# Optimization experiments

Measured on AMD Instinct MI355X. Metric: run time of the kernel, lower is better.

## Reference

```python
import jax, jax.numpy as jnp
import numpy as np

INPUT_DIM = 512
HIDDEN_DIM = 1024


def glorot_normal(key, shape):
    fan_in, fan_out = shape[0], shape[1]
    std = jnp.sqrt(2.0 / (fan_in + fan_out))
    return std * jax.random.normal(key, shape, dtype=jnp.float32)


def setup_inputs() -> dict:
    key = jax.random.key(0)
    k1, k2, k3 = jax.random.split(key, 3)
    b, t = 32, 1024
    H = HIDDEN_DIM + INPUT_DIM
    x_btd = jax.random.normal(k1, (b, t, INPUT_DIM), dtype=jnp.float32)
    input_paddings = jnp.zeros((b, t), dtype=jnp.float32)
    kernel = glorot_normal(k2, (H, 4 * HIDDEN_DIM))  # [H, 4h]
    bias = jnp.zeros((4 * HIDDEN_DIM,), dtype=jnp.float32)
    h_init = glorot_normal(k3, (1, HIDDEN_DIM))
    return {"x_btd": x_btd, "input_paddings": input_paddings,
            "kernel": kernel, "bias": bias, "h_init": h_init}


def lstm_step(carry, x_bd, kernel, bias):
    h_bh, c_bh = carry
    x_bH = jnp.concatenate([x_bd, h_bh], axis=-1)          # [b, d+h]
    gate_out = jnp.einsum('bH,Hh->bh', x_bH, kernel) + bias  # [b, 4h]
    f, i, o, g = jnp.split(gate_out, 4, axis=-1)
    c_new = jax.nn.sigmoid(f) * c_bh + jax.nn.sigmoid(i) * jnp.tanh(g)
    h_new = jax.nn.sigmoid(o) * jnp.tanh(c_new)
    return (h_new, c_new), h_new


def reference(x_btd, input_paddings, kernel, bias, h_init) -> jnp.ndarray:
    del input_paddings
    b = x_btd.shape[0]
    h0 = jnp.tile(h_init, (b, 1))                # [b, h]
    c0 = jnp.zeros((b, HIDDEN_DIM), dtype=x_btd.dtype)
    x_tbd = jnp.transpose(x_btd, (1, 0, 2))      # [t, b, d]

    def step(carry, x_bd):
        return lstm_step(carry, x_bd, kernel, bias)

    _, h_tbh = jax.lax.scan(step, (h0, c0), x_tbd)
    return jnp.transpose(h_tbh, (1, 0, 2))       # [b, t, h]
```

## Files before the change

### kernel.cpp

```cpp
#include <hip/hip_runtime.h>


#define T_STEPS 1024
#define BATCH   32
#define DIN     512
#define HID     1024
#define KTOT    1536
#define NBLK    128
#define RSTR    68
#define REDW    (16*RSTR)
#define NSLOT   8
#define HSLOT   32768

typedef __attribute__((ext_vector_type(8))) short  short8;
typedef __attribute__((ext_vector_type(4))) float  floatx4;
typedef __attribute__((ext_vector_type(4))) unsigned int uintx4;
typedef __attribute__((ext_vector_type(4))) unsigned short ushort4_;

#define MFMA16(a,b,c) __builtin_amdgcn_mfma_f32_16x16x32_bf16(a, b, c, 0, 0, 0)

__device__ __forceinline__ unsigned short f2bf(float f) {
    unsigned u = __builtin_bit_cast(unsigned, f);
    u += 0x7FFFu + ((u >> 16) & 1u);
    return (unsigned short)(u >> 16);
}
__device__ __forceinline__ float sigf(float x) { return 1.f / (1.f + __expf(-x)); }
__device__ __forceinline__ float tanh_fast(float x) {
    float e = __expf(2.f * x);
    return 1.f - 2.f / (e + 1.f);
}
__device__ __forceinline__ unsigned cvt2(float a, float b) {
    unsigned r;
    asm("v_cvt_pk_bf16_f32 %0, %1, %2" : "=v"(r) : "v"(a), "v"(b));
    return r;
}

__device__ __forceinline__ floatx4 coh_load16f(const void* p) {
    floatx4 v;
    asm volatile("global_load_dwordx4 %0, %1, off sc1" : "=v"(v) : "v"(p));
    return v;
}
__device__ __forceinline__ void coh_store4u(void* p, unsigned v) {
    asm volatile("global_store_dword %0, %1, off sc1" :: "v"(p), "v"(v) : "memory");
}
__device__ __forceinline__ void wait_vm0() {
    asm volatile("s_waitcnt vmcnt(0)" ::: "memory");
}

__global__ __launch_bounds__(256) void prep_wt(const float* __restrict__ kern,
                                               unsigned short* __restrict__ wt) {
    __shared__ unsigned short tile[64][72];
    const int c0 = (blockIdx.x & 63) * 64;
    const int k0 = (blockIdx.x >> 6) * 64;
    const int cl = threadIdx.x & 63;
    const int kg = threadIdx.x >> 6;
    #pragma unroll
    for (int i = 0; i < 16; ++i) {
        int kl = kg * 16 + i;
        tile[cl][kl] = f2bf(kern[(k0 + kl) * 4096 + c0 + cl]);
    }
    __syncthreads();
    #pragma unroll
    for (int i = 0; i < 16; ++i) {
        int cc = kg * 16 + i;
        wt[(size_t)(c0 + cc) * KTOT + k0 + cl] = tile[cc][cl];
    }
}

__global__ __launch_bounds__(256) void prep_x(const float* __restrict__ x,
                                              unsigned short* __restrict__ xT) {
    const int row = blockIdx.x * 2 + (threadIdx.x >> 7);
    const int l   = threadIdx.x & 127;
    const int b = row >> 10, t = row & 1023;
    float4 v = ((const float4*)(x + (size_t)row * DIN))[l];
    ushort4_ o;
    o.x = f2bf(v.x); o.y = f2bf(v.y); o.z = f2bf(v.z); o.w = f2bf(v.w);
    *(ushort4_*)(xT + ((size_t)t * BATCH + b) * DIN + l * 4) = o;
}

__global__ __launch_bounds__(256) void init_h(const float* __restrict__ h_init,
                                              unsigned* __restrict__ hbuf_u) {
    const int idx = blockIdx.x * 256 + threadIdx.x;
    const int uu = idx & 1023;
    hbuf_u[idx] = __builtin_bit_cast(unsigned, h_init[uu]) & ~1u;
    hbuf_u[HSLOT + idx] = 1u;
}

__global__ __launch_bounds__(512, 2) void lstm_persist(
    const unsigned short* __restrict__ wt,
    const unsigned short* __restrict__ xT,
    float* __restrict__ hbuf,
    const float* __restrict__ bias,
    float* __restrict__ out)
{
    __shared__ float red[2][NSLOT][REDW];

    const int bk   = blockIdx.x;
    const int p    = bk >> 6;
    const int ug   = bk & 63;
    const int tid  = threadIdx.x;
    const int w    = tid >> 6;
    const int lane = tid & 63;
    const int lrow = lane & 15;
    const int kq   = lane >> 4;

    unsigned* hbuf_u = (unsigned*)hbuf;

    short8 wbx[2][4], wbh[4][4];
    #pragma unroll
    for (int nf = 0; nf < 4; ++nf) {
        const size_t gcol = (size_t)(nf * HID + ug * 16 + lrow) * KTOT;
        #pragma unroll
        for (int i = 0; i < 2; ++i)
            wbx[i][nf] = *(const short8*)(wt + gcol + w * 64 + i * 32 + kq * 8);
        #pragma unroll
        for (int j = 0; j < 4; ++j)
            wbh[j][nf] = *(const short8*)(wt + gcol + 512 + w * 128 + j * 32 + kq * 8);
    }

    const int pb = tid >> 4;
    const int pu = tid & 15;
    float bias_r[4], c_state = 0.f;
    if (tid < 256) {
        #pragma unroll
        for (int g = 0; g < 4; ++g) bias_r[g] = bias[g * HID + ug * 16 + pu];
    }

    const int hoff = (p * 16 + lrow) * HID + w * 128 + kq * 8;

    floatx4 xa[2];

    {
        const floatx4 zero = {0.f, 0.f, 0.f, 0.f};
        floatx4 acc[4] = {zero, zero, zero, zero};
        const unsigned short* xb = xT + (size_t)(p * 16 + lrow) * DIN;
        #pragma unroll
        for (int i = 0; i < 2; ++i) {
            short8 a = *(const short8*)(xb + w * 64 + i * 32 + kq * 8);
            #pragma unroll
            for (int nf = 0; nf < 4; ++nf) acc[nf] = MFMA16(a, wbx[i][nf], acc[nf]);
        }
        const unsigned short* xn = xT + ((size_t)1 * BATCH + p * 16 + lrow) * DIN;
        #pragma unroll
        for (int i = 0; i < 2; ++i)
            xa[i] = *(const floatx4*)(xn + w * 64 + i * 32 + kq * 8);

        floatx4 hf[4][2];
        #pragma unroll
        for (int j = 0; j < 4; ++j) {
            hf[j][0] = coh_load16f(hbuf + hoff + j * 32);
            hf[j][1] = coh_load16f(hbuf + hoff + j * 32 + 4);
        }
        wait_vm0();
        __builtin_amdgcn_sched_barrier(0);
        #pragma unroll
        for (int j = 0; j < 4; ++j) {
            union { short8 s; unsigned u[4]; } wa;
            wa.u[0] = cvt2(hf[j][0][0], hf[j][0][1]);
            wa.u[1] = cvt2(hf[j][0][2], hf[j][0][3]);
            wa.u[2] = cvt2(hf[j][1][0], hf[j][1][1]);
            wa.u[3] = cvt2(hf[j][1][2], hf[j][1][3]);
            #pragma unroll
            for (int nf = 0; nf < 4; ++nf) acc[nf] = MFMA16(wa.s, wbh[j][nf], acc[nf]);
        }
        #pragma unroll
        for (int nf = 0; nf < 4; ++nf)
            #pragma unroll
            for (int r = 0; r < 4; ++r)
                red[0][w][(kq * 4 + r) * RSTR + nf * 16 + lrow] = acc[nf][r];
    }

    for (int t = 0; t < T_STEPS; ++t) {
        __syncthreads();

        const float* rc = &red[t & 1][0][0];
        float*       rn = &red[(t + 1) & 1][0][0];
        const unsigned tg = ((unsigned)(t + 1) >> 1) & 1u;
        const int      so = ((t + 1) & 1) * HSLOT;

        if (tid < 256) {
            float gv[4];
            #pragma unroll
            for (int g = 0; g < 4; ++g) {
                float s = bias_r[g];
                #pragma unroll
                for (int wv = 0; wv < NSLOT; ++wv)
                    s += rc[wv * REDW + pb * RSTR + g * 16 + pu];
                gv[g] = s;
            }
            const float fg = sigf(gv[0]);
            const float ig = sigf(gv[1]);
            const float og = sigf(gv[2]);
            const float gg = tanh_fast(gv[3]);
            c_state = fg * c_state + ig * gg;
            const float hn = og * tanh_fast(c_state);

            if (t + 1 < T_STEPS) {
                wait_vm0();
                unsigned hv = (__builtin_bit_cast(unsigned, hn) & ~1u) | tg;
                coh_store4u(hbuf_u + so + (p * 16 + pb) * HID + ug * 16 + pu, hv);
            }
            out[(size_t)(p * 16 + pb) * (T_STEPS * HID) + (size_t)t * HID
                + ug * 16 + pu] = hn;
        }

        if (t + 1 == T_STEPS) break;

        const floatx4 zero = {0.f, 0.f, 0.f, 0.f};
        floatx4 acc[4] = {zero, zero, zero, zero};
        #pragma unroll
        for (int i = 0; i < 2; ++i) {
            short8 a = __builtin_bit_cast(short8, xa[i]);
            #pragma unroll
            for (int nf = 0; nf < 4; ++nf) acc[nf] = MFMA16(a, wbx[i][nf], acc[nf]);
        }
        if (t + 2 < T_STEPS) {
            const unsigned short* xn = xT + ((size_t)(t + 2) * BATCH + p * 16 + lrow) * DIN;
            #pragma unroll
            for (int i = 0; i < 2; ++i)
                xa[i] = *(const floatx4*)(xn + w * 64 + i * 32 + kq * 8);
        }

        if (tid >= 256) __builtin_amdgcn_s_sleep(12);
        const float* hb = hbuf + so + hoff;
        floatx4 hf[4][2];
        #pragma unroll
        for (int j = 0; j < 4; ++j) {
            hf[j][0] = coh_load16f(hb + j * 32);
            hf[j][1] = coh_load16f(hb + j * 32 + 4);
        }
        wait_vm0();
        __builtin_amdgcn_sched_barrier(0);
        unsigned stale = 0;
        #pragma unroll
        for (int j = 0; j < 4; ++j)
            #pragma unroll
            for (int c2 = 0; c2 < 2; ++c2) {
                uintx4 u = __builtin_bit_cast(uintx4, hf[j][c2]);
                unsigned fr = tg ? (u[0] & u[1] & u[2] & u[3])
                                 : ~(u[0] | u[1] | u[2] | u[3]);
                if (!(fr & 1u)) stale |= 1u << (j * 2 + c2);
            }
        while (__any((int)(stale != 0u))) {
            if (__all((int)(stale == 0xFFu)))
                __builtin_amdgcn_s_sleep(8);
            #pragma unroll
            for (int j = 0; j < 4; ++j)
                #pragma unroll
                for (int c2 = 0; c2 < 2; ++c2)
                    if (stale & (1u << (j * 2 + c2)))
                        hf[j][c2] = coh_load16f(hb + j * 32 + c2 * 4);
            wait_vm0();
            __builtin_amdgcn_sched_barrier(0);
            unsigned ns = 0;
            #pragma unroll
            for (int j = 0; j < 4; ++j)
                #pragma unroll
                for (int c2 = 0; c2 < 2; ++c2)
                    if (stale & (1u << (j * 2 + c2))) {
                        uintx4 u = __builtin_bit_cast(uintx4, hf[j][c2]);
                        unsigned fr = tg ? (u[0] & u[1] & u[2] & u[3])
                                         : ~(u[0] | u[1] | u[2] | u[3]);
                        if (!(fr & 1u)) ns |= 1u << (j * 2 + c2);
                    }
            stale = ns;
        }

        #pragma unroll
        for (int j = 0; j < 4; ++j) {
            union { short8 s; unsigned u[4]; } wa;
            wa.u[0] = cvt2(hf[j][0][0], hf[j][0][1]);
            wa.u[1] = cvt2(hf[j][0][2], hf[j][0][3]);
            wa.u[2] = cvt2(hf[j][1][0], hf[j][1][1]);
            wa.u[3] = cvt2(hf[j][1][2], hf[j][1][3]);
            #pragma unroll
            for (int nf = 0; nf < 4; ++nf) acc[nf] = MFMA16(wa.s, wbh[j][nf], acc[nf]);
        }

        #pragma unroll
        for (int nf = 0; nf < 4; ++nf)
            #pragma unroll
            for (int r = 0; r < 4; ++r)
                rn[w * REDW + (kq * 4 + r) * RSTR + nf * 16 + lrow] = acc[nf][r];
    }
}

extern "C" void kernel_launch(void* const* d_in, const int* in_sizes, int n_in,
                              void* d_out, int out_size, void* d_ws, size_t ws_size,
                              hipStream_t stream) {
    (void)in_sizes; (void)n_in; (void)out_size;
    const float* x      = (const float*)d_in[0];
    const float* kern   = (const float*)d_in[2];
    const float* bias   = (const float*)d_in[3];
    const float* h_init = (const float*)d_in[4];
    float* out = (float*)d_out;

    char* ws = (char*)d_ws;
    unsigned short* wt   = (unsigned short*)(ws);
    unsigned short* xT   = (unsigned short*)(ws + 12582912);
    float*          hbuf = (float*)(ws + 12582912 + 33554432);
    (void)ws_size;

    prep_wt<<<dim3(64 * 24), dim3(256), 0, stream>>>(kern, wt);
    prep_x<<<dim3(BATCH * T_STEPS / 2), dim3(256), 0, stream>>>(x, xT);
    init_h<<<dim3(128), dim3(256), 0, stream>>>(h_init, (unsigned*)hbuf);

    void* args[] = { &wt, &xT, &hbuf, &bias, &out };
    hipLaunchCooperativeKernel((const void*)lstm_persist, dim3(NBLK), dim3(512),
                               args, 0, stream);
}
```

Before: 5.227 ms.

## Specialize waves into input-projection and recurrent-polling groups with adaptive backoff

Splits the eight waves per block into two roles. Four waves compute only the x·W input projection with doubled K depth, and four waves handle the h·W recurrent part, polling the coherent h buffer with doubled K depth. The point is to take the x projection and x prefetch off the critical polling path and to replace the fixed sleep with an adaptive backoff sized by how many polling rounds were needed. It also drops the wait before the h store and lowers launch bounds to one block per SIMD-group, which allows more registers per wave for the larger weight tile. The catch is that the h waves now do twice the MFMA work on the serial critical path.

```diff
diff --git a/kernel.cpp b/kernel.cpp
--- a/kernel.cpp
+++ b/kernel.cpp
@@ -86,7 +86,7 @@
     hbuf_u[HSLOT + idx] = 1u;
 }
 
-__global__ __launch_bounds__(512, 2) void lstm_persist(
+__global__ __launch_bounds__(512, 1) void lstm_persist(
     const unsigned short* __restrict__ wt,
     const unsigned short* __restrict__ xT,
     float* __restrict__ hbuf,
@@ -99,23 +99,32 @@
     const int p    = bk >> 6;
     const int ug   = bk & 63;
     const int tid  = threadIdx.x;
-    const int w    = tid >> 6;
+    const int wave = tid >> 6;
     const int lane = tid & 63;
     const int lrow = lane & 15;
     const int kq   = lane >> 4;
+    const bool isG = wave < 4;
 
     unsigned* hbuf_u = (unsigned*)hbuf;
 
-    short8 wbx[2][4], wbh[4][4];
-    #pragma unroll
-    for (int nf = 0; nf < 4; ++nf) {
-        const size_t gcol = (size_t)(nf * HID + ug * 16 + lrow) * KTOT;
+    short8 wb[8][4];
+    if (isG) {
         #pragma unroll
-        for (int i = 0; i < 2; ++i)
-            wbx[i][nf] = *(const short8*)(wt + gcol + w * 64 + i * 32 + kq * 8);
+        for (int nf = 0; nf < 4; ++nf) {
+            const size_t gcol = (size_t)(nf * HID + ug * 16 + lrow) * KTOT;
+            #pragma unroll
+            for (int i = 0; i < 4; ++i)
+                wb[i][nf] = *(const short8*)(wt + gcol + wave * 128 + i * 32 + kq * 8);
+        }
+    } else {
+        const int wh = wave - 4;
         #pragma unroll
-        for (int j = 0; j < 4; ++j)
-            wbh[j][nf] = *(const short8*)(wt + gcol + 512 + w * 128 + j * 32 + kq * 8);
+        for (int nf = 0; nf < 4; ++nf) {
+            const size_t gcol = (size_t)(nf * HID + ug * 16 + lrow) * KTOT;
+            #pragma unroll
+            for (int j = 0; j < 8; ++j)
+                wb[j][nf] = *(const short8*)(wt + gcol + 512 + wh * 256 + j * 32 + kq * 8);
+        }
     }
 
     const int pb = tid >> 4;
@@ -126,49 +135,53 @@
         for (int g = 0; g < 4; ++g) bias_r[g] = bias[g * HID + ug * 16 + pu];
     }
 
-    const int hoff = (p * 16 + lrow) * HID + w * 128 + kq * 8;
-
-    floatx4 xa[2];
+    const int hoff = (p * 16 + lrow) * HID + (wave - 4) * 256 + kq * 8;
+
+    floatx4 xa[4];
 
     {
         const floatx4 zero = {0.f, 0.f, 0.f, 0.f};
         floatx4 acc[4] = {zero, zero, zero, zero};
-        const unsigned short* xb = xT + (size_t)(p * 16 + lrow) * DIN;
-        #pragma unroll
-        for (int i = 0; i < 2; ++i) {
-            short8 a = *(const short8*)(xb + w * 64 + i * 32 + kq * 8);
-            #pragma unroll
-            for (int nf = 0; nf < 4; ++nf) acc[nf] = MFMA16(a, wbx[i][nf], acc[nf]);
-        }
-        const unsigned short* xn = xT + ((size_t)1 * BATCH + p * 16 + lrow) * DIN;
-        #pragma unroll
-        for (int i = 0; i < 2; ++i)
-            xa[i] = *(const floatx4*)(xn + w * 64 + i * 32 + kq * 8);
-
-        floatx4 hf[4][2];
-        #pragma unroll
-        for (int j = 0; j < 4; ++j) {
-            hf[j][0] = coh_load16f(hbuf + hoff + j * 32);
-            hf[j][1] = coh_load16f(hbuf + hoff + j * 32 + 4);
-        }
-        wait_vm0();
-        __builtin_amdgcn_sched_barrier(0);
-        #pragma unroll
-        for (int j = 0; j < 4; ++j) {
-            union { short8 s; unsigned u[4]; } wa;
-            wa.u[0] = cvt2(hf[j][0][0], hf[j][0][1]);
-            wa.u[1] = cvt2(hf[j][0][2], hf[j][0][3]);
-            wa.u[2] = cvt2(hf[j][1][0], hf[j][1][1]);
-            wa.u[3] = cvt2(hf[j][1][2], hf[j][1][3]);
-            #pragma unroll
-            for (int nf = 0; nf < 4; ++nf) acc[nf] = MFMA16(wa.s, wbh[j][nf], acc[nf]);
+        if (isG) {
+            const unsigned short* xb = xT + (size_t)(p * 16 + lrow) * DIN;
+            #pragma unroll
+            for (int i = 0; i < 4; ++i) {
+                short8 a = *(const short8*)(xb + wave * 128 + i * 32 + kq * 8);
+                #pragma unroll
+                for (int nf = 0; nf < 4; ++nf) acc[nf] = MFMA16(a, wb[i][nf], acc[nf]);
+            }
+            const unsigned short* xn = xT + ((size_t)1 * BATCH + p * 16 + lrow) * DIN;
+            #pragma unroll
+            for (int i = 0; i < 4; ++i)
+                xa[i] = *(const floatx4*)(xn + wave * 128 + i * 32 + kq * 8);
+        } else {
+            floatx4 hf[8][2];
+            #pragma unroll
+            for (int j = 0; j < 8; ++j) {
+                hf[j][0] = coh_load16f(hbuf + hoff + j * 32);
+                hf[j][1] = coh_load16f(hbuf + hoff + j * 32 + 4);
+            }
+            wait_vm0();
+            __builtin_amdgcn_sched_barrier(0);
+            #pragma unroll
+            for (int j = 0; j < 8; ++j) {
+                union { short8 s; unsigned u[4]; } wa;
+                wa.u[0] = cvt2(hf[j][0][0], hf[j][0][1]);
+                wa.u[1] = cvt2(hf[j][0][2], hf[j][0][3]);
+                wa.u[2] = cvt2(hf[j][1][0], hf[j][1][1]);
+                wa.u[3] = cvt2(hf[j][1][2], hf[j][1][3]);
+                #pragma unroll
+                for (int nf = 0; nf < 4; ++nf) acc[nf] = MFMA16(wa.s, wb[j][nf], acc[nf]);
+            }
         }
         #pragma unroll
         for (int nf = 0; nf < 4; ++nf)
             #pragma unroll
             for (int r = 0; r < 4; ++r)
-                red[0][w][(kq * 4 + r) * RSTR + nf * 16 + lrow] = acc[nf][r];
-    }
+                red[0][wave][(kq * 4 + r) * RSTR + nf * 16 + lrow] = acc[nf][r];
+    }
+
+    int slp = 8;
 
     for (int t = 0; t < T_STEPS; ++t) {
         __syncthreads();
@@ -196,7 +209,6 @@
             const float hn = og * tanh_fast(c_state);
 
             if (t + 1 < T_STEPS) {
-                wait_vm0();
                 unsigned hv = (__builtin_bit_cast(unsigned, hn) & ~1u) | tg;
                 coh_store4u(hbuf_u + so + (p * 16 + pb) * HID + ug * 16 + pu, hv);
             }
@@ -208,80 +220,90 @@
 
         const floatx4 zero = {0.f, 0.f, 0.f, 0.f};
         floatx4 acc[4] = {zero, zero, zero, zero};
-        #pragma unroll
-        for (int i = 0; i < 2; ++i) {
-            short8 a = __builtin_bit_cast(short8, xa[i]);
-            #pragma unroll
-            for (int nf = 0; nf < 4; ++nf) acc[nf] = MFMA16(a, wbx[i][nf], acc[nf]);
-        }
-        if (t + 2 < T_STEPS) {
-            const unsigned short* xn = xT + ((size_t)(t + 2) * BATCH + p * 16 + lrow) * DIN;
-            #pragma unroll
-            for (int i = 0; i < 2; ++i)
-                xa[i] = *(const floatx4*)(xn + w * 64 + i * 32 + kq * 8);
-        }
-
-        if (tid >= 256) __builtin_amdgcn_s_sleep(12);
-        const float* hb = hbuf + so + hoff;
-        floatx4 hf[4][2];
-        #pragma unroll
-        for (int j = 0; j < 4; ++j) {
-            hf[j][0] = coh_load16f(hb + j * 32);
-            hf[j][1] = coh_load16f(hb + j * 32 + 4);
-        }
-        wait_vm0();
-        __builtin_amdgcn_sched_barrier(0);
-        unsigned stale = 0;
-        #pragma unroll
-        for (int j = 0; j < 4; ++j)
-            #pragma unroll
-            for (int c2 = 0; c2 < 2; ++c2) {
-                uintx4 u = __builtin_bit_cast(uintx4, hf[j][c2]);
-                unsigned fr = tg ? (u[0] & u[1] & u[2] & u[3])
-                                 : ~(u[0] | u[1] | u[2] | u[3]);
-                if (!(fr & 1u)) stale |= 1u << (j * 2 + c2);
-            }
-        while (__any((int)(stale != 0u))) {
-            if (__all((int)(stale == 0xFFu)))
-                __builtin_amdgcn_s_sleep(8);
-            #pragma unroll
-            for (int j = 0; j < 4; ++j)
-                #pragma unroll
-                for (int c2 = 0; c2 < 2; ++c2)
-                    if (stale & (1u << (j * 2 + c2)))
-                        hf[j][c2] = coh_load16f(hb + j * 32 + c2 * 4);
+
+        if (isG) {
+            #pragma unroll
+            for (int i = 0; i < 4; ++i) {
+                short8 a = __builtin_bit_cast(short8, xa[i]);
+                #pragma unroll
+                for (int nf = 0; nf < 4; ++nf) acc[nf] = MFMA16(a, wb[i][nf], acc[nf]);
+            }
+            #pragma unroll
+            for (int nf = 0; nf < 4; ++nf)
+                #pragma unroll
+                for (int r = 0; r < 4; ++r)
+                    rn[wave * REDW + (kq * 4 + r) * RSTR + nf * 16 + lrow] = acc[nf][r];
+            if (t + 2 < T_STEPS) {
+                const unsigned short* xn =
+                    xT + ((size_t)(t + 2) * BATCH + p * 16 + lrow) * DIN;
+                #pragma unroll
+                for (int i = 0; i < 4; ++i)
+                    xa[i] = *(const floatx4*)(xn + wave * 128 + i * 32 + kq * 8);
+            }
+        } else {
+            for (int s = slp; s > 0; --s) __builtin_amdgcn_s_sleep(1);
+            const float* hb = hbuf + so + hoff;
+            floatx4 hf[8][2];
+            #pragma unroll
+            for (int j = 0; j < 8; ++j) {
+                hf[j][0] = coh_load16f(hb + j * 32);
+                hf[j][1] = coh_load16f(hb + j * 32 + 4);
+            }
             wait_vm0();
             __builtin_amdgcn_sched_barrier(0);
-            unsigned ns = 0;
-            #pragma unroll
-            for (int j = 0; j < 4; ++j)
-                #pragma unroll
-                for (int c2 = 0; c2 < 2; ++c2)
-                    if (stale & (1u << (j * 2 + c2))) {
-                        uintx4 u = __builtin_bit_cast(uintx4, hf[j][c2]);
-                        unsigned fr = tg ? (u[0] & u[1] & u[2] & u[3])
-                                         : ~(u[0] | u[1] | u[2] | u[3]);
-                        if (!(fr & 1u)) ns |= 1u << (j * 2 + c2);
-                    }
-            stale = ns;
-        }
-
-        #pragma unroll
-        for (int j = 0; j < 4; ++j) {
-            union { short8 s; unsigned u[4]; } wa;
-            wa.u[0] = cvt2(hf[j][0][0], hf[j][0][1]);
-            wa.u[1] = cvt2(hf[j][0][2], hf[j][0][3]);
-            wa.u[2] = cvt2(hf[j][1][0], hf[j][1][1]);
-            wa.u[3] = cvt2(hf[j][1][2], hf[j][1][3]);
-            #pragma unroll
-            for (int nf = 0; nf < 4; ++nf) acc[nf] = MFMA16(wa.s, wbh[j][nf], acc[nf]);
-        }
-
-        #pragma unroll
-        for (int nf = 0; nf < 4; ++nf)
-            #pragma unroll
-            for (int r = 0; r < 4; ++r)
-                rn[w * REDW + (kq * 4 + r) * RSTR + nf * 16 + lrow] = acc[nf][r];
+            unsigned stale = 0;
+            #pragma unroll
+            for (int j = 0; j < 8; ++j)
+                #pragma unroll
+                for (int c2 = 0; c2 < 2; ++c2) {
+                    uintx4 u = __builtin_bit_cast(uintx4, hf[j][c2]);
+                    unsigned fr = tg ? (u[0] & u[1] & u[2] & u[3])
+                                     : ~(u[0] | u[1] | u[2] | u[3]);
+                    if (!(fr & 1u)) stale |= 1u << (j * 2 + c2);
+                }
+            int rounds = 1;
+            while (__any((int)(stale != 0u))) {
+                ++rounds;
+                #pragma unroll
+                for (int j = 0; j < 8; ++j)
+                    #pragma unroll
+                    for (int c2 = 0; c2 < 2; ++c2)
+                        if (stale & (1u << (j * 2 + c2)))
+                            hf[j][c2] = coh_load16f(hb + j * 32 + c2 * 4);
+                wait_vm0();
+                __builtin_amdgcn_sched_barrier(0);
+                unsigned ns = 0;
+                #pragma unroll
+                for (int j = 0; j < 8; ++j)
+                    #pragma unroll
+                    for (int c2 = 0; c2 < 2; ++c2)
+                        if (stale & (1u << (j * 2 + c2))) {
+                            uintx4 u = __builtin_bit_cast(uintx4, hf[j][c2]);
+                            unsigned fr = tg ? (u[0] & u[1] & u[2] & u[3])
+                                             : ~(u[0] | u[1] | u[2] | u[3]);
+                            if (!(fr & 1u)) ns |= 1u << (j * 2 + c2);
+                        }
+                stale = ns;
+            }
+            if (rounds == 1) { if (slp > 0) --slp; }
+            else { slp += 2 * (rounds - 1); if (slp > 48) slp = 48; }
+
+            #pragma unroll
+            for (int j = 0; j < 8; ++j) {
+                union { short8 s; unsigned u[4]; } wa;
+                wa.u[0] = cvt2(hf[j][0][0], hf[j][0][1]);
+                wa.u[1] = cvt2(hf[j][0][2], hf[j][0][3]);
+                wa.u[2] = cvt2(hf[j][1][0], hf[j][1][1]);
+                wa.u[3] = cvt2(hf[j][1][2], hf[j][1][3]);
+                #pragma unroll
+                for (int nf = 0; nf < 4; ++nf) acc[nf] = MFMA16(wa.s, wb[j][nf], acc[nf]);
+            }
+            #pragma unroll
+            for (int nf = 0; nf < 4; ++nf)
+                #pragma unroll
+                for (int r = 0; r < 4; ++r)
+                    rn[wave * REDW + (kq * 4 + r) * RSTR + nf * 16 + lrow] = acc[nf][r];
+        }
     }
 }
 
```

Result: slower. 7.056 ms (+35.0%).
